# Kernel tuning notes

Hardware: AMD Instinct MI355X
Metric: run time of the kernel (lower is better)

Reference implementation:

```python
import jax, jax.numpy as jnp
import numpy as np

# PyTorch LSTM gate order: i, f, g, o. Dropout layers are identity in eval mode.

def _lstm_step(w_ih, w_hh, b):
    def step(carry, xt):
        h, c = carry
        g = xt @ w_ih.T + h @ w_hh.T + b
        i, f, gg, o = jnp.split(g, 4, axis=-1)
        c = jax.nn.sigmoid(f) * c + jax.nn.sigmoid(i) * jnp.tanh(gg)
        h = jax.nn.sigmoid(o) * jnp.tanh(c)
        return (h, c), h
    return step


def bilstm(x, wf_ih, wf_hh, bf_ih, bf_hh, wb_ih, wb_hh, bb_ih, bb_hh):
    # x: [B, T, D] -> out: [B, T, 2H]
    B = x.shape[0]
    H = wf_hh.shape[1]
    xt = jnp.swapaxes(x, 0, 1)  # [T, B, D]
    init = (jnp.zeros((B, H), x.dtype), jnp.zeros((B, H), x.dtype))
    _, hf = jax.lax.scan(_lstm_step(wf_ih, wf_hh, bf_ih + bf_hh), init, xt)
    _, hb = jax.lax.scan(_lstm_step(wb_ih, wb_hh, bb_ih + bb_hh), init, xt[::-1])
    hb = hb[::-1]
    return jnp.swapaxes(jnp.concatenate([hf, hb], axis=-1), 0, 1)


def setup_inputs() -> dict:
    key = jax.random.key(0)
    ks = iter(jax.random.split(key, 64))
    d = {"x": jax.random.normal(next(ks), (1024, 1024, 8), jnp.float32)}
    layer_dims = [(16, 20), (40, 20), (40, 10), (20, 10)]
    for li, (din, H) in enumerate(layer_dims, start=1):
        for dr in ("f", "b"):
            d[f"w{li}{dr}_ih"] = 0.1 * jax.random.normal(next(ks), (4 * H, din), jnp.float32)
            d[f"w{li}{dr}_hh"] = 0.1 * jax.random.normal(next(ks), (4 * H, H), jnp.float32)
            d[f"b{li}{dr}_ih"] = 0.1 * jax.random.normal(next(ks), (4 * H,), jnp.float32)
            d[f"b{li}{dr}_hh"] = 0.1 * jax.random.normal(next(ks), (4 * H,), jnp.float32)
    d["fc_w"] = 0.1 * jax.random.normal(next(ks), (1, 20), jnp.float32)
    d["fc_b"] = 0.1 * jax.random.normal(next(ks), (1,), jnp.float32)
    return d


def reference(x,
              w1f_ih, w1f_hh, b1f_ih, b1f_hh, w1b_ih, w1b_hh, b1b_ih, b1b_hh,
              w2f_ih, w2f_hh, b2f_ih, b2f_hh, w2b_ih, w2b_hh, b2b_ih, b2b_hh,
              w3f_ih, w3f_hh, b3f_ih, b3f_hh, w3b_ih, w3b_hh, b3b_ih, b3b_hh,
              w4f_ih, w4f_hh, b4f_ih, b4f_hh, w4b_ih, w4b_hh, b4b_ih, b4b_hh,
              fc_w, fc_b):
    # lag-1 concat: [B,T,8] -> [B,T,16]
    x_lag = jnp.concatenate([jnp.zeros_like(x[:, :1, :]), x[:, :-1, :]], axis=1)
    h = jnp.concatenate([x, x_lag], axis=2)
    h = bilstm(h, w1f_ih, w1f_hh, b1f_ih, b1f_hh, w1b_ih, w1b_hh, b1b_ih, b1b_hh)
    h = bilstm(h, w2f_ih, w2f_hh, b2f_ih, b2f_hh, w2b_ih, w2b_hh, b2b_ih, b2b_hh)
    h = bilstm(h, w3f_ih, w3f_hh, b3f_ih, b3f_hh, w3b_ih, w3b_hh, b3b_ih, b3b_hh)
    h = bilstm(h, w4f_ih, w4f_hh, b4f_ih, b4f_hh, w4b_ih, w4b_hh, b4b_ih, b4b_hh)
    h = h[:, -1, :]  # [B, 20]
    return jax.nn.sigmoid(h @ fc_w.T + fc_b)
```

## Files before the change

kernel.cpp:

```cpp
#include <hip/hip_runtime.h>
#include <hip/hip_fp16.h>
#include <stdint.h>

#define B_TOTAL 1024
#define T_TOTAL 1024
#define LOG2E 1.44269504088896f

typedef _Float16 f16x2 __attribute__((ext_vector_type(2)));

__device__ __forceinline__ float dot2acc(uint32_t xw, f16x2 w, float acc) {
#if __has_builtin(__builtin_amdgcn_fdot2)
    return __builtin_amdgcn_fdot2(__builtin_bit_cast(f16x2, xw), w, acc, false);
#else
    f16x2 xv = __builtin_bit_cast(f16x2, xw);
    return acc + (float)xv.x * (float)w.x + (float)xv.y * (float)w.y;
#endif
}

__device__ __forceinline__ uint32_t packf2(float a, float b) {
    f16x2 t;
    t.x = (_Float16)a;
    t.y = (_Float16)b;
    return __builtin_bit_cast(uint32_t, t);
}

__device__ __forceinline__ float sigm_(float z) {
    float e = __builtin_amdgcn_exp2f(-LOG2E * z);
    return __builtin_amdgcn_rcpf(1.0f + e);
}
__device__ __forceinline__ float tanh_(float z) {
    float e = __builtin_amdgcn_exp2f((2.0f * LOG2E) * z);
    float r = __builtin_amdgcn_rcpf(1.0f + e);
    return __builtin_fmaf(-2.0f, r, 1.0f);
}

__device__ __forceinline__ void wavebar() {
#if __has_builtin(__builtin_amdgcn_wave_barrier)
    __builtin_amdgcn_wave_barrier();
#endif
}

template <int DIN, int H, int NDIR, int GPB, bool LAYER1, bool STORE_ALL>
__global__ void __launch_bounds__(64, 1) lstm_fused(
    const float* __restrict__ x,
    const __half* __restrict__ inbuf,
    const float* __restrict__ wihf, const float* __restrict__ whhf,
    const float* __restrict__ bihf, const float* __restrict__ bhhf,
    const float* __restrict__ wihb, const float* __restrict__ whhb,
    const float* __restrict__ bihb, const float* __restrict__ bhhb,
    __half* __restrict__ outbuf,
    float* __restrict__ lasth)
{
    constexpr int LPG = NDIR * H;
    constexpr int NL  = GPB * LPG;
    constexpr int ND  = DIN / 2;
    constexpr int NH  = H / 2;
    constexpr int NHL = NH / 2;
    constexpr int HSP = (NH + 3) & ~3;

    const int lane = threadIdx.x;
    const bool act = lane < NL;
    const int la   = act ? lane : 0;
    const int g    = la / LPG;
    const int rr   = la % LPG;
    const int dir  = (NDIR == 2) ? (rr / H) : 0;
    const int j    = (NDIR == 2) ? (rr % H) : rr;
    const int b    = blockIdx.x * GPB + g;
    const int sgn  = dir ? -1 : 1;
    int tt         = dir ? (T_TOTAL - 1) : 0;

    const float* w_ih = dir ? wihb : wihf;
    const float* w_hh = dir ? whhb : whhf;
    const float* b_ih = dir ? bihb : bihf;
    const float* b_hh = dir ? bhhb : bhhf;

    __shared__ uint32_t hsm[GPB][NDIR][HSP];
    uint32_t* hrow = &hsm[g][dir][0];
    __half*   hhlf = (__half*)hrow;

    f16x2 whh2[4][NH];
    float bias[4];
#pragma unroll
    for (int q = 0; q < 4; ++q) {
        const int r_ = q * H + j;
#pragma unroll
        for (int k = 0; k < NH; ++k) {
            f16x2 t;
            t.x = (_Float16)w_hh[r_ * H + 2 * k];
            t.y = (_Float16)w_hh[r_ * H + 2 * k + 1];
            whh2[q][k] = t;
        }
        bias[q] = b_ih[r_] + b_hh[r_];
    }

    float wih1[LAYER1 ? 64 : 1];
    f16x2 wih2[LAYER1 ? 1 : 4][LAYER1 ? 1 : ND];
    if constexpr (LAYER1) {
#pragma unroll
        for (int q = 0; q < 4; ++q)
#pragma unroll
            for (int i = 0; i < 16; ++i)
                wih1[q * 16 + i] = w_ih[(q * H + j) * 16 + i];
    } else {
#pragma unroll
        for (int q = 0; q < 4; ++q) {
            const int r_ = q * H + j;
#pragma unroll
            for (int d = 0; d < ND; ++d) {
                f16x2 t;
                t.x = (_Float16)w_ih[r_ * DIN + 2 * d];
                t.y = (_Float16)w_ih[r_ * DIN + 2 * d + 1];
                wih2[q][d] = t;
            }
        }
    }

    __half* op = nullptr;
    ptrdiff_t opstep = 0;
    if constexpr (STORE_ALL) {
        op = outbuf + ((size_t)tt * B_TOTAL + b) * (2 * H) + dir * H + j;
        opstep = (ptrdiff_t)sgn * (B_TOTAL * 2 * H);
    }

    float c = 0.0f, h = 0.0f;
    if (act) hhlf[j] = __float2half(0.0f);
    wavebar();

    auto finish = [&](const float* xl, const float* xh) {
        uint32_t hd[NH];
#pragma unroll
        for (int k = 0; k < NH; ++k) hd[k] = hrow[k];
        float hl[4] = {0, 0, 0, 0}, hh[4] = {0, 0, 0, 0};
#pragma unroll
        for (int k = 0; k < NHL; ++k)
#pragma unroll
            for (int q = 0; q < 4; ++q) hl[q] = dot2acc(hd[k], whh2[q][k], hl[q]);
#pragma unroll
        for (int k = NHL; k < NH; ++k)
#pragma unroll
            for (int q = 0; q < 4; ++q) hh[q] = dot2acc(hd[k], whh2[q][k], hh[q]);
        const float a0 = (xl[0] + xh[0]) + (hl[0] + hh[0]);
        const float a1 = (xl[1] + xh[1]) + (hl[1] + hh[1]);
        const float a2 = (xl[2] + xh[2]) + (hl[2] + hh[2]);
        const float a3 = (xl[3] + xh[3]) + (hl[3] + hh[3]);
        const float iv = sigm_(a0);
        const float fv = sigm_(a1);
        const float gv = tanh_(a2);
        const float ov = sigm_(a3);
        c = __builtin_fmaf(fv, c, iv * gv);
        h = ov * tanh_(c);
        if (act) hhlf[j] = __float2half(h);
        wavebar();
        if constexpr (STORE_ALL) {
            if (act) *op = __float2half(h);
            op += opstep;
        }
    };

    if constexpr (LAYER1) {
        const float* xrow = x + (size_t)b * (T_TOTAL * 8);
        float xcur[8], xlag[8];
        {
            const float* p = xrow + (size_t)tt * 8;
#pragma unroll
            for (int i = 0; i < 8; ++i) xcur[i] = p[i];
            const float* q = xrow + (size_t)(tt - (dir ? 1 : 0)) * 8;
#pragma unroll
            for (int i = 0; i < 8; ++i) xlag[i] = dir ? q[i] : 0.0f;
        }
        for (int t = 0; t < T_TOTAL; ++t) {
            float xl[4], xh[4];
#pragma unroll
            for (int q = 0; q < 4; ++q) {
                float a = bias[q], bsum = 0.0f;
#pragma unroll
                for (int i = 0; i < 8; ++i) {
                    a    = __builtin_fmaf(wih1[q * 16 + i],     xcur[i], a);
                    bsum = __builtin_fmaf(wih1[q * 16 + 8 + i], xlag[i], bsum);
                }
                xl[q] = a; xh[q] = bsum;
            }
            const int li = dir ? (tt - 2) : (tt + 1);
            const bool ld = (li >= 0) && (li < T_TOTAL);
            float np[8];
            if (ld) {
                const float* p = xrow + (size_t)li * 8;
#pragma unroll
                for (int i = 0; i < 8; ++i) np[i] = p[i];
            } else {
#pragma unroll
                for (int i = 0; i < 8; ++i) np[i] = 0.0f;
            }
            finish(xl, xh);
#pragma unroll
            for (int i = 0; i < 8; ++i) {
                const float nc = dir ? xlag[i] : np[i];
                const float nl = dir ? np[i]   : xcur[i];
                xcur[i] = nc; xlag[i] = nl;
            }
            tt += sgn;
        }
    } else {
        const ptrdiff_t ipstep = (ptrdiff_t)sgn * (B_TOTAL * ND);
        const uint32_t* ip = (const uint32_t*)inbuf + ((size_t)tt * B_TOTAL + b) * ND;

        auto loadrow = [&](uint32_t* dst) {
            if constexpr ((ND % 4) == 0) {
#pragma unroll
                for (int q4 = 0; q4 < ND / 4; ++q4) {
                    uint4 v = ((const uint4*)ip)[q4];
                    dst[4 * q4] = v.x; dst[4 * q4 + 1] = v.y;
                    dst[4 * q4 + 2] = v.z; dst[4 * q4 + 3] = v.w;
                }
            } else {
#pragma unroll
                for (int q2 = 0; q2 < ND / 2; ++q2) {
                    uint2 v = ((const uint2*)ip)[q2];
                    dst[2 * q2] = v.x; dst[2 * q2 + 1] = v.y;
                }
                if constexpr (ND & 1) dst[ND - 1] = ip[ND - 1];
            }
            ip += ipstep;
        };

        uint32_t xb[4][ND];
#pragma unroll
        for (int s = 0; s < 3; ++s) loadrow(xb[s]);

        auto step = [&](const uint32_t* xc, uint32_t* xn, bool pf) {
            float xl[4], xh[4];
#pragma unroll
            for (int q = 0; q < 4; ++q) { xl[q] = bias[q]; xh[q] = 0.0f; }
#pragma unroll
            for (int d = 0; d < ND / 2; ++d)
#pragma unroll
                for (int q = 0; q < 4; ++q) xl[q] = dot2acc(xc[d], wih2[q][d], xl[q]);
#pragma unroll
            for (int d = ND / 2; d < ND; ++d)
#pragma unroll
                for (int q = 0; q < 4; ++q) xh[q] = dot2acc(xc[d], wih2[q][d], xh[q]);
            if (pf) loadrow(xn);
            finish(xl, xh);
            tt += sgn;
        };

        for (int t = 0; t < T_TOTAL; t += 4) {
            step(xb[0], xb[3], t + 3 < T_TOTAL);
            step(xb[1], xb[0], t + 4 < T_TOTAL);
            step(xb[2], xb[1], t + 5 < T_TOTAL);
            step(xb[3], xb[2], t + 6 < T_TOTAL);
        }
    }

    if constexpr (!STORE_ALL) {
        if (act) lasth[b * H + j] = h;
    }
}

__global__ void final_kernel(const __half* __restrict__ l3out,
                             const float* __restrict__ hf4,
                             const float* __restrict__ w_ih,
                             const float* __restrict__ b_ih,
                             const float* __restrict__ b_hh,
                             const float* __restrict__ fc_w,
                             const float* __restrict__ fc_b,
                             float* __restrict__ out)
{
    const int b = blockIdx.x * blockDim.x + threadIdx.x;
    if (b >= B_TOTAL) return;

    float in4[20];
    const __half* p = l3out + (size_t)(T_TOTAL - 1) * (B_TOTAL * 20) + (size_t)b * 20;
#pragma unroll
    for (int i = 0; i < 20; ++i) in4[i] = __half2float(p[i]);

    float z = fc_b[0];
#pragma unroll
    for (int k = 0; k < 10; ++k) z += fc_w[k] * hf4[b * 10 + k];

#pragma unroll
    for (int k = 0; k < 10; ++k) {
        float gi = b_ih[k]      + b_hh[k];
        float gg = b_ih[20 + k] + b_hh[20 + k];
        float go = b_ih[30 + k] + b_hh[30 + k];
#pragma unroll
        for (int i = 0; i < 20; ++i) {
            const float xi = in4[i];
            gi += w_ih[k * 20 + i]        * xi;
            gg += w_ih[(20 + k) * 20 + i] * xi;
            go += w_ih[(30 + k) * 20 + i] * xi;
        }
        const float cc = sigm_(gi) * tanh_(gg);
        const float hb = sigm_(go) * tanh_(cc);
        z += fc_w[10 + k] * hb;
    }
    out[b] = sigm_(z);
}

extern "C" void kernel_launch(void* const* d_in, const int* in_sizes, int n_in,
                              void* d_out, int out_size, void* d_ws, size_t ws_size,
                              hipStream_t stream) {
    const float* x = (const float*)d_in[0];
    auto W = [&](int li, int dr, int k) -> const float* {
        return (const float*)d_in[1 + (li - 1) * 8 + dr * 4 + k];
    };
    const float* fc_w = (const float*)d_in[33];
    const float* fc_b = (const float*)d_in[34];
    float* out = (float*)d_out;

    constexpr size_t MB = 1ull << 20;
    char* w8 = (char*)d_ws;
    __half* A0  = (__half*)w8;
    __half* A1  = (__half*)(w8 + 80 * MB);
    float*  HF4 = (float*)(w8 + 160 * MB);

    lstm_fused<16, 20, 2, 1, true, true><<<1024, 64, 0, stream>>>(
        x, nullptr,
        W(1,0,0), W(1,0,1), W(1,0,2), W(1,0,3),
        W(1,1,0), W(1,1,1), W(1,1,2), W(1,1,3),
        A0, nullptr);

    lstm_fused<40, 20, 2, 1, false, true><<<1024, 64, 0, stream>>>(
        nullptr, A0,
        W(2,0,0), W(2,0,1), W(2,0,2), W(2,0,3),
        W(2,1,0), W(2,1,1), W(2,1,2), W(2,1,3),
        A1, nullptr);

    lstm_fused<40, 10, 2, 1, false, true><<<1024, 64, 0, stream>>>(
        nullptr, A1,
        W(3,0,0), W(3,0,1), W(3,0,2), W(3,0,3),
        W(3,1,0), W(3,1,1), W(3,1,2), W(3,1,3),
        A0, nullptr);

    lstm_fused<20, 10, 1, 2, false, false><<<512, 64, 0, stream>>>(
        nullptr, A0,
        W(4,0,0), W(4,0,1), W(4,0,2), W(4,0,3),
        W(4,0,0), W(4,0,1), W(4,0,2), W(4,0,3),
        nullptr, HF4);

    final_kernel<<<dim3(4, 1, 1), 256, 0, stream>>>(
        A0, HF4, W(4,1,0), W(4,1,2), W(4,1,3), fc_w, fc_b, out);
}
```

Before: 2.016 ms.

## Replace per-lane dot2 LSTM recurrence with MFMA over 16-sequence batch tiles

The LSTM kernels are rewritten so each 64-lane wave handles 16 batch sequences of one direction and computes the gate pre-activations with 16x16x32 f16 MFMA instructions, with inputs and hidden state staged in LDS. Blocks drop from 1024 per layer to 128 (or 64 for the last layer), which cuts the number of waves but puts much more work on each one. The input for upcoming timesteps is staged into a 4-slot LDS ring ahead of use. The risks are MFMA latency on the serial recurrence chain, fewer active CUs, and padding waste when H is 10 or 20.

Result: slower. 4.396 ms (+118.0%).

```diff
diff --git a/kernel.cpp b/kernel.cpp
--- a/kernel.cpp
+++ b/kernel.cpp
@@ -7,15 +7,8 @@
 #define LOG2E 1.44269504088896f
 
 typedef _Float16 f16x2 __attribute__((ext_vector_type(2)));
-
-__device__ __forceinline__ float dot2acc(uint32_t xw, f16x2 w, float acc) {
-#if __has_builtin(__builtin_amdgcn_fdot2)
-    return __builtin_amdgcn_fdot2(__builtin_bit_cast(f16x2, xw), w, acc, false);
-#else
-    f16x2 xv = __builtin_bit_cast(f16x2, xw);
-    return acc + (float)xv.x * (float)w.x + (float)xv.y * (float)w.y;
-#endif
-}
+typedef _Float16 f16x8 __attribute__((ext_vector_type(8)));
+typedef float    f32x4 __attribute__((ext_vector_type(4)));
 
 __device__ __forceinline__ uint32_t packf2(float a, float b) {
     f16x2 t;
@@ -40,8 +33,12 @@
 #endif
 }
 
-template <int DIN, int H, int NDIR, int GPB, bool LAYER1, bool STORE_ALL>
-__global__ void __launch_bounds__(64, 1) lstm_fused(
+__device__ __forceinline__ f32x4 mfma16(f16x8 a, f16x8 b, f32x4 c) {
+    return __builtin_amdgcn_mfma_f32_16x16x32_f16(a, b, c, 0, 0, 0);
+}
+
+template <int D, int H, bool LAYER1, bool STORE_ALL>
+__global__ void __launch_bounds__(64, 1) lstm_mfma(
     const float* __restrict__ x,
     const __half* __restrict__ inbuf,
     const float* __restrict__ wihf, const float* __restrict__ whhf,
@@ -51,209 +48,179 @@
     __half* __restrict__ outbuf,
     float* __restrict__ lasth)
 {
-    constexpr int LPG = NDIR * H;
-    constexpr int NL  = GPB * LPG;
-    constexpr int ND  = DIN / 2;
-    constexpr int NH  = H / 2;
-    constexpr int NHL = NH / 2;
-    constexpr int HSP = (NH + 3) & ~3;
-
-    const int lane = threadIdx.x;
-    const bool act = lane < NL;
-    const int la   = act ? lane : 0;
-    const int g    = la / LPG;
-    const int rr   = la % LPG;
-    const int dir  = (NDIR == 2) ? (rr / H) : 0;
-    const int j    = (NDIR == 2) ? (rr % H) : rr;
-    const int b    = blockIdx.x * GPB + g;
+    constexpr int UT = (H + 15) / 16;
+    constexpr int KT = (D + 31) / 32;
+    constexpr int XP = KT * 32;
+
+    const int dir  = blockIdx.y;
+    const int l    = threadIdx.x;
+    const int quad = l >> 4;
+    const int ln   = l & 15;
+    const int b0   = blockIdx.x * 16;
     const int sgn  = dir ? -1 : 1;
-    int tt         = dir ? (T_TOTAL - 1) : 0;
+    const int tt0  = dir ? (T_TOTAL - 1) : 0;
 
     const float* w_ih = dir ? wihb : wihf;
     const float* w_hh = dir ? whhb : whhf;
     const float* b_ih = dir ? bihb : bihf;
     const float* b_hh = dir ? bhhb : bhhf;
 
-    __shared__ uint32_t hsm[GPB][NDIR][HSP];
-    uint32_t* hrow = &hsm[g][dir][0];
-    __half*   hhlf = (__half*)hrow;
-
-    f16x2 whh2[4][NH];
-    float bias[4];
+    __shared__ __align__(16) __half hA[16][32];
+    __shared__ __align__(16) __half xA[4][16][XP];
+
+    {
+        uint32_t* z1 = (uint32_t*)&hA[0][0];
+#pragma unroll
+        for (int i = 0; i < (16 * 32 / 2) / 64; ++i) z1[l + 64 * i] = 0u;
+        uint32_t* z2 = (uint32_t*)&xA[0][0][0];
+        constexpr int ZN = 4 * 16 * XP / 2;
+#pragma unroll
+        for (int i = 0; i < ZN / 64; ++i) z2[l + 64 * i] = 0u;
+    }
+    wavebar();
+
+    f16x8 Bx[4][UT][KT];
+    f16x8 Bh[4][UT];
+    float bias[4][UT];
 #pragma unroll
     for (int q = 0; q < 4; ++q) {
-        const int r_ = q * H + j;
-#pragma unroll
-        for (int k = 0; k < NH; ++k) {
-            f16x2 t;
-            t.x = (_Float16)w_hh[r_ * H + 2 * k];
-            t.y = (_Float16)w_hh[r_ * H + 2 * k + 1];
-            whh2[q][k] = t;
-        }
-        bias[q] = b_ih[r_] + b_hh[r_];
-    }
-
-    float wih1[LAYER1 ? 64 : 1];
-    f16x2 wih2[LAYER1 ? 1 : 4][LAYER1 ? 1 : ND];
+#pragma unroll
+        for (int ut = 0; ut < UT; ++ut) {
+            const int u  = ut * 16 + ln;
+            const bool uv = (u < H);
+            const int r  = q * H + (uv ? u : 0);
+#pragma unroll
+            for (int kt = 0; kt < KT; ++kt) {
+#pragma unroll
+                for (int e = 0; e < 8; ++e) {
+                    const int kg = kt * 32 + quad * 8 + e;
+                    const float wv = (uv && kg < D) ? w_ih[r * D + kg] : 0.0f;
+                    Bx[q][ut][kt][e] = (_Float16)wv;
+                }
+            }
+#pragma unroll
+            for (int e = 0; e < 8; ++e) {
+                const int kg = quad * 8 + e;
+                const float wv = (uv && kg < H) ? w_hh[r * H + kg] : 0.0f;
+                Bh[q][ut][e] = (_Float16)wv;
+            }
+            bias[q][ut] = uv ? (b_ih[r] + b_hh[r]) : 0.0f;
+        }
+    }
+
+    const float2* xp = nullptr;
+    const uint32_t* sp = nullptr;
     if constexpr (LAYER1) {
+        xp = (const float2*)(x + ((size_t)(b0 + (l >> 2)) * T_TOTAL + tt0) * 8) + (l & 3);
+    } else {
+        sp = (const uint32_t*)inbuf + ((size_t)tt0 * B_TOTAL + b0) * (D / 2);
+    }
+
+    auto stage = [&](int ts) {
+        const bool ok = (ts >= 0) && (ts < T_TOTAL);
+        if constexpr (LAYER1) {
+            float2 v = {0.0f, 0.0f};
+            if (ok) v = *xp;
+            xp += sgn * 4;
+            if (ok) {
+                const uint32_t dw = packf2(v.x, v.y);
+                const int row = l >> 2, pos = (l & 3) * 2;
+                *(uint32_t*)&xA[ts & 3][row][pos] = dw;
+                if (ts + 1 < T_TOTAL)
+                    *(uint32_t*)&xA[(ts + 1) & 3][row][8 + pos] = dw;
+                if (ts == 0)
+                    *(uint32_t*)&xA[0][row][8 + pos] = 0u;
+            }
+        } else {
+            constexpr int TD = 16 * D / 2;
+            if (ok) {
+#pragma unroll
+                for (int it = 0; it < (TD + 63) / 64; ++it) {
+                    const int i = l + 64 * it;
+                    if (TD % 64 == 0 || i < TD) {
+                        const uint32_t dw = sp[i];
+                        const int row = (2 * i) / D;
+                        const int col = (2 * i) % D;
+                        *(uint32_t*)&xA[ts & 3][row][col] = dw;
+                    }
+                }
+            }
+            sp += (ptrdiff_t)sgn * (B_TOTAL * (D / 2));
+        }
+    };
+
+    stage(tt0);
+    stage(tt0 + sgn);
+
+    float cst[UT][4];
+#pragma unroll
+    for (int ut = 0; ut < UT; ++ut)
+#pragma unroll
+        for (int r = 0; r < 4; ++r) cst[ut][r] = 0.0f;
+
+    __half* op = nullptr;
+    if constexpr (STORE_ALL) {
+        op = outbuf + ((size_t)tt0 * B_TOTAL + (b0 + quad * 4)) * (2 * H) + dir * H + ln;
+    }
+
+    int tt = tt0;
+    for (int t = 0; t < T_TOTAL; ++t) {
+        stage(tt + 2 * sgn);
+
+        f32x4 acc[4][UT];
 #pragma unroll
         for (int q = 0; q < 4; ++q)
 #pragma unroll
-            for (int i = 0; i < 16; ++i)
-                wih1[q * 16 + i] = w_ih[(q * H + j) * 16 + i];
-    } else {
-#pragma unroll
-        for (int q = 0; q < 4; ++q) {
-            const int r_ = q * H + j;
-#pragma unroll
-            for (int d = 0; d < ND; ++d) {
-                f16x2 t;
-                t.x = (_Float16)w_ih[r_ * DIN + 2 * d];
-                t.y = (_Float16)w_ih[r_ * DIN + 2 * d + 1];
-                wih2[q][d] = t;
-            }
-        }
-    }
-
-    __half* op = nullptr;
-    ptrdiff_t opstep = 0;
-    if constexpr (STORE_ALL) {
-        op = outbuf + ((size_t)tt * B_TOTAL + b) * (2 * H) + dir * H + j;
-        opstep = (ptrdiff_t)sgn * (B_TOTAL * 2 * H);
-    }
-
-    float c = 0.0f, h = 0.0f;
-    if (act) hhlf[j] = __float2half(0.0f);
-    wavebar();
-
-    auto finish = [&](const float* xl, const float* xh) {
-        uint32_t hd[NH];
-#pragma unroll
-        for (int k = 0; k < NH; ++k) hd[k] = hrow[k];
-        float hl[4] = {0, 0, 0, 0}, hh[4] = {0, 0, 0, 0};
-#pragma unroll
-        for (int k = 0; k < NHL; ++k)
-#pragma unroll
-            for (int q = 0; q < 4; ++q) hl[q] = dot2acc(hd[k], whh2[q][k], hl[q]);
-#pragma unroll
-        for (int k = NHL; k < NH; ++k)
-#pragma unroll
-            for (int q = 0; q < 4; ++q) hh[q] = dot2acc(hd[k], whh2[q][k], hh[q]);
-        const float a0 = (xl[0] + xh[0]) + (hl[0] + hh[0]);
-        const float a1 = (xl[1] + xh[1]) + (hl[1] + hh[1]);
-        const float a2 = (xl[2] + xh[2]) + (hl[2] + hh[2]);
-        const float a3 = (xl[3] + xh[3]) + (hl[3] + hh[3]);
-        const float iv = sigm_(a0);
-        const float fv = sigm_(a1);
-        const float gv = tanh_(a2);
-        const float ov = sigm_(a3);
-        c = __builtin_fmaf(fv, c, iv * gv);
-        h = ov * tanh_(c);
-        if (act) hhlf[j] = __float2half(h);
+            for (int ut = 0; ut < UT; ++ut) {
+                const float bv = bias[q][ut];
+                acc[q][ut][0] = bv; acc[q][ut][1] = bv;
+                acc[q][ut][2] = bv; acc[q][ut][3] = bv;
+            }
+#pragma unroll
+        for (int kt = 0; kt < KT; ++kt) {
+            const f16x8 ax = *(const f16x8*)&xA[tt & 3][ln][kt * 32 + quad * 8];
+#pragma unroll
+            for (int q = 0; q < 4; ++q)
+#pragma unroll
+                for (int ut = 0; ut < UT; ++ut)
+                    acc[q][ut] = mfma16(ax, Bx[q][ut][kt], acc[q][ut]);
+        }
         wavebar();
-        if constexpr (STORE_ALL) {
-            if (act) *op = __float2half(h);
-            op += opstep;
-        }
-    };
-
-    if constexpr (LAYER1) {
-        const float* xrow = x + (size_t)b * (T_TOTAL * 8);
-        float xcur[8], xlag[8];
         {
-            const float* p = xrow + (size_t)tt * 8;
-#pragma unroll
-            for (int i = 0; i < 8; ++i) xcur[i] = p[i];
-            const float* q = xrow + (size_t)(tt - (dir ? 1 : 0)) * 8;
-#pragma unroll
-            for (int i = 0; i < 8; ++i) xlag[i] = dir ? q[i] : 0.0f;
-        }
-        for (int t = 0; t < T_TOTAL; ++t) {
-            float xl[4], xh[4];
-#pragma unroll
-            for (int q = 0; q < 4; ++q) {
-                float a = bias[q], bsum = 0.0f;
-#pragma unroll
-                for (int i = 0; i < 8; ++i) {
-                    a    = __builtin_fmaf(wih1[q * 16 + i],     xcur[i], a);
-                    bsum = __builtin_fmaf(wih1[q * 16 + 8 + i], xlag[i], bsum);
+            const f16x8 ah = *(const f16x8*)&hA[ln][quad * 8];
+#pragma unroll
+            for (int q = 0; q < 4; ++q)
+#pragma unroll
+                for (int ut = 0; ut < UT; ++ut)
+                    acc[q][ut] = mfma16(ah, Bh[q][ut], acc[q][ut]);
+        }
+        wavebar();
+
+#pragma unroll
+        for (int ut = 0; ut < UT; ++ut) {
+            const int u = ut * 16 + ln;
+#pragma unroll
+            for (int r = 0; r < 4; ++r) {
+                const float iv = sigm_(acc[0][ut][r]);
+                const float fv = sigm_(acc[1][ut][r]);
+                const float gv = tanh_(acc[2][ut][r]);
+                const float ov = sigm_(acc[3][ut][r]);
+                cst[ut][r] = __builtin_fmaf(fv, cst[ut][r], iv * gv);
+                const float hv = ov * tanh_(cst[ut][r]);
+                const int row = quad * 4 + r;
+                if (u < H) {
+                    hA[row][u] = __float2half(hv);
+                    if constexpr (STORE_ALL) {
+                        op[r * 2 * H + ut * 16] = __float2half(hv);
+                    } else {
+                        if (t == T_TOTAL - 1)
+                            lasth[(size_t)(b0 + row) * H + u] = hv;
+                    }
                 }
-                xl[q] = a; xh[q] = bsum;
-            }
-            const int li = dir ? (tt - 2) : (tt + 1);
-            const bool ld = (li >= 0) && (li < T_TOTAL);
-            float np[8];
-            if (ld) {
-                const float* p = xrow + (size_t)li * 8;
-#pragma unroll
-                for (int i = 0; i < 8; ++i) np[i] = p[i];
-            } else {
-#pragma unroll
-                for (int i = 0; i < 8; ++i) np[i] = 0.0f;
-            }
-            finish(xl, xh);
-#pragma unroll
-            for (int i = 0; i < 8; ++i) {
-                const float nc = dir ? xlag[i] : np[i];
-                const float nl = dir ? np[i]   : xcur[i];
-                xcur[i] = nc; xlag[i] = nl;
-            }
-            tt += sgn;
-        }
-    } else {
-        const ptrdiff_t ipstep = (ptrdiff_t)sgn * (B_TOTAL * ND);
-        const uint32_t* ip = (const uint32_t*)inbuf + ((size_t)tt * B_TOTAL + b) * ND;
-
-        auto loadrow = [&](uint32_t* dst) {
-            if constexpr ((ND % 4) == 0) {
-#pragma unroll
-                for (int q4 = 0; q4 < ND / 4; ++q4) {
-                    uint4 v = ((const uint4*)ip)[q4];
-                    dst[4 * q4] = v.x; dst[4 * q4 + 1] = v.y;
-                    dst[4 * q4 + 2] = v.z; dst[4 * q4 + 3] = v.w;
-                }
-            } else {
-#pragma unroll
-                for (int q2 = 0; q2 < ND / 2; ++q2) {
-                    uint2 v = ((const uint2*)ip)[q2];
-                    dst[2 * q2] = v.x; dst[2 * q2 + 1] = v.y;
-                }
-                if constexpr (ND & 1) dst[ND - 1] = ip[ND - 1];
-            }
-            ip += ipstep;
-        };
-
-        uint32_t xb[4][ND];
-#pragma unroll
-        for (int s = 0; s < 3; ++s) loadrow(xb[s]);
-
-        auto step = [&](const uint32_t* xc, uint32_t* xn, bool pf) {
-            float xl[4], xh[4];
-#pragma unroll
-            for (int q = 0; q < 4; ++q) { xl[q] = bias[q]; xh[q] = 0.0f; }
-#pragma unroll
-            for (int d = 0; d < ND / 2; ++d)
-#pragma unroll
-                for (int q = 0; q < 4; ++q) xl[q] = dot2acc(xc[d], wih2[q][d], xl[q]);
-#pragma unroll
-            for (int d = ND / 2; d < ND; ++d)
-#pragma unroll
-                for (int q = 0; q < 4; ++q) xh[q] = dot2acc(xc[d], wih2[q][d], xh[q]);
-            if (pf) loadrow(xn);
-            finish(xl, xh);
-            tt += sgn;
-        };
-
-        for (int t = 0; t < T_TOTAL; t += 4) {
-            step(xb[0], xb[3], t + 3 < T_TOTAL);
-            step(xb[1], xb[0], t + 4 < T_TOTAL);
-            step(xb[2], xb[1], t + 5 < T_TOTAL);
-            step(xb[3], xb[2], t + 6 < T_TOTAL);
-        }
-    }
-
-    if constexpr (!STORE_ALL) {
-        if (act) lasth[b * H + j] = h;
+            }
+        }
+        if constexpr (STORE_ALL) op += (ptrdiff_t)sgn * (B_TOTAL * 2 * H);
+        tt += sgn;
     }
 }
 
@@ -314,25 +281,25 @@
     __half* A1  = (__half*)(w8 + 80 * MB);
     float*  HF4 = (float*)(w8 + 160 * MB);
 
-    lstm_fused<16, 20, 2, 1, true, true><<<1024, 64, 0, stream>>>(
+    lstm_mfma<16, 20, true, true><<<dim3(64, 2), 64, 0, stream>>>(
         x, nullptr,
         W(1,0,0), W(1,0,1), W(1,0,2), W(1,0,3),
         W(1,1,0), W(1,1,1), W(1,1,2), W(1,1,3),
         A0, nullptr);
 
-    lstm_fused<40, 20, 2, 1, false, true><<<1024, 64, 0, stream>>>(
+    lstm_mfma<40, 20, false, true><<<dim3(64, 2), 64, 0, stream>>>(
         nullptr, A0,
         W(2,0,0), W(2,0,1), W(2,0,2), W(2,0,3),
         W(2,1,0), W(2,1,1), W(2,1,2), W(2,1,3),
         A1, nullptr);
 
-    lstm_fused<40, 10, 2, 1, false, true><<<1024, 64, 0, stream>>>(
+    lstm_mfma<40, 10, false, true><<<dim3(64, 2), 64, 0, stream>>>(
         nullptr, A1,
         W(3,0,0), W(3,0,1), W(3,0,2), W(3,0,3),
         W(3,1,0), W(3,1,1), W(3,1,2), W(3,1,3),
         A0, nullptr);
 
-    lstm_fused<20, 10, 1, 2, false, false><<<512, 64, 0, stream>>>(
+    lstm_mfma<20, 10, false, false><<<dim3(64, 1), 64, 0, stream>>>(
         nullptr, A0,
         W(4,0,0), W(4,0,1), W(4,0,2), W(4,0,3),
         W(4,0,0), W(4,0,1), W(4,0,2), W(4,0,3),
```
